# Performance work log

Hardware: AMD Instinct MI355X
Metric: run time of the kernel (lower is better)

Reference implementation:

```python
import jax, jax.numpy as jnp
import numpy as np

ALPHA = 1000.0


def setup_inputs() -> dict:
    key = jax.random.key(0)
    ks = jax.random.split(key, 5)
    B, D_in, K = 8192, 2048, 256  # K = n_clusters = embed_dim (square cluster_reps)
    x = jax.random.normal(ks[0], (B, D_in), dtype=jnp.float32)
    W_enc = jax.random.normal(ks[1], (D_in, K), dtype=jnp.float32) * (1.0 / np.sqrt(D_in))
    b_enc = jnp.zeros((K,), dtype=jnp.float32)
    W_dec = jax.random.normal(ks[2], (K, D_in), dtype=jnp.float32) * (1.0 / np.sqrt(K))
    b_dec = jnp.zeros((D_in,), dtype=jnp.float32)
    cluster_reps = jax.random.normal(ks[3], (K, K), dtype=jnp.float32)
    return {"x": x, "W_enc": W_enc, "b_enc": b_enc, "W_dec": W_dec,
            "b_dec": b_dec, "cluster_reps": cluster_reps}


def reference(x, W_enc, b_enc, W_dec, b_dec, cluster_reps):
    # Autoencoder (linear MLP stand-in for the injected module)
    emb = x @ W_enc + b_enc                    # [B, K]
    reconstruction = emb @ W_dec + b_dec       # [B, D_in]

    # Squared Euclidean distance to each cluster rep, in GEMM form: [B, K]
    # dist[b, k] = ||emb_b||^2 - 2 emb_b . c_k + ||c_k||^2
    dist = (jnp.sum(emb * emb, axis=1, keepdims=True)
            - 2.0 * (emb @ cluster_reps.T)
            + jnp.sum(cluster_reps * cluster_reps, axis=1)[None, :])

    stack_dist = dist.T                        # [K, B] (matches torch.stack over clusters)
    min_dist = jnp.min(stack_dist, axis=0)     # [B]
    stack_exp = jnp.exp(-ALPHA * (stack_dist - min_dist[None, :]))  # stable softmin
    softmax = stack_exp / jnp.sum(stack_exp, axis=0, keepdims=True)
    weighted_dist = stack_dist * softmax       # [K, B]
    return weighted_dist, reconstruction
```

## Files before the change

kernel.cpp:

```cpp
#include <hip/hip_runtime.h>

#define ALPHA_F 1000.0f

typedef _Float16 half8 __attribute__((ext_vector_type(8)));
typedef float floatx4 __attribute__((ext_vector_type(4)));

__global__ __launch_bounds__(256) void prep(
    const float* __restrict__ W_enc, const float* __restrict__ W_dec,
    const float* __restrict__ creps,
    _Float16* __restrict__ Wh, _Float16* __restrict__ Wl,
    _Float16* __restrict__ Wdh,
    _Float16* __restrict__ Ch, _Float16* __restrict__ Cl,
    float* __restrict__ cnorm)
{
    const int bid = blockIdx.x;
    if (bid < 256) {
        const int q = bid * 256 + threadIdx.x;
        const int n = q & 255, k8 = q >> 8;
        const int k = k8 * 8;
        half8 h, l;
        #pragma unroll
        for (int i = 0; i < 8; ++i) {
            const float v = W_enc[(size_t)(k + i) * 256 + n] * 256.0f;
            const _Float16 hi = (_Float16)v;
            h[i] = hi;
            l[i] = (_Float16)(v - (float)hi);
        }
        const int kc = k >> 5, nt = n >> 4;
        const int lane = (n & 15) | ((k8 & 3) << 4);
        const size_t idx = (size_t)((kc * 16 + nt) * 64 + lane) * 8;
        *(half8*)(Wh + idx) = h;
        *(half8*)(Wl + idx) = l;
    } else if (bid < 512) {
        const int q = (bid - 256) * 256 + threadIdx.x;
        const int n = q & 2047, k8 = q >> 11;
        const int k = k8 * 8;
        half8 h;
        #pragma unroll
        for (int i = 0; i < 8; ++i) h[i] = (_Float16)W_dec[(size_t)(k + i) * 2048 + n];
        const int kc = k8 >> 2, nt = n >> 4;
        const int lane = (n & 15) | ((k8 & 3) << 4);
        *(half8*)(Wdh + (size_t)((kc * 128 + nt) * 64 + lane) * 8) = h;
    } else if (bid < 544) {
        const int q = (bid - 512) * 256 + threadIdx.x;
        const int n = q & 255, j8 = q >> 8;
        const int j = j8 * 8;
        half8 h, l;
        #pragma unroll
        for (int i = 0; i < 8; ++i) {
            const float v = creps[(size_t)n * 256 + j + i];
            const _Float16 hi = (_Float16)v;
            h[i] = hi;
            l[i] = (_Float16)((v - (float)hi) * 2048.0f);
        }
        const int jc = j >> 5, nt = n >> 4;
        const int lane = (n & 15) | ((j8 & 3) << 4);
        const size_t idx = (size_t)((jc * 16 + nt) * 64 + lane) * 8;
        *(half8*)(Ch + idx) = h;
        *(half8*)(Cl + idx) = l;
    } else {
        const int wid = threadIdx.x >> 6, lane = threadIdx.x & 63;
        const int row = (bid - 544) * 4 + wid;
        const float4 v = *(const float4*)(creps + (size_t)row * 256 + lane * 4);
        float s = v.x * v.x + v.y * v.y + v.z * v.z + v.w * v.w;
        #pragma unroll
        for (int off = 32; off >= 1; off >>= 1) s += __shfl_xor(s, off, 64);
        if (lane == 0) cnorm[row] = s;
    }
}

__global__ __launch_bounds__(256) void emb_gemm(
    const float* __restrict__ x, const _Float16* __restrict__ Wh,
    const _Float16* __restrict__ Wl, float* __restrict__ P)
{
    __shared__ _Float16 Ah[2][2048], Al[2][2048];
    const int t = threadIdx.x, lane = t & 63, w = t >> 6;
    const int kk = blockIdx.x;
    const int mb = blockIdx.y;
    const int m0 = mb * 64;

    const int am = t >> 2, q = t & 3;
    const int aoff = (((am >> 4) * 64) + ((am & 15) | (q << 4))) * 8;
    const float* xP = x + (size_t)(m0 + am) * 2048 + kk * 512 + q * 8;

    const _Float16* bhP = Wh + (size_t)((kk * 256 + w * 4) * 64 + lane) * 8;
    const _Float16* blP = Wl + (size_t)((kk * 256 + w * 4) * 64 + lane) * 8;

    floatx4 acc[4][4] = {};
    half8 bh[4], bl[4];

    {
        const float4 v0 = *(const float4*)(xP);
        const float4 v1 = *(const float4*)(xP + 4);
        const float vv[8] = {v0.x, v0.y, v0.z, v0.w, v1.x, v1.y, v1.z, v1.w};
        half8 h8, l8;
        #pragma unroll
        for (int i = 0; i < 8; ++i) {
            const _Float16 hi = (_Float16)vv[i];
            h8[i] = hi;
            l8[i] = (_Float16)(vv[i] - (float)hi);
        }
        *(half8*)(&Ah[0][aoff]) = h8;
        *(half8*)(&Al[0][aoff]) = l8;
        #pragma unroll
        for (int ni = 0; ni < 4; ++ni) {
            bh[ni] = *(const half8*)(bhP + ni * 512);
            bl[ni] = *(const half8*)(blP + ni * 512);
        }
        asm volatile("s_waitcnt lgkmcnt(0)" ::: "memory");
        __builtin_amdgcn_sched_barrier(0);
        __builtin_amdgcn_s_barrier();
    }

    #pragma unroll 2
    for (int it = 0; it < 16; ++it) {
        const int buf = it & 1;

        float4 n0, n1;
        half8 nbh[4], nbl[4];
        if (it < 15) {
            n0 = *(const float4*)(xP + (it + 1) * 32);
            n1 = *(const float4*)(xP + (it + 1) * 32 + 4);
            #pragma unroll
            for (int ni = 0; ni < 4; ++ni) {
                nbh[ni] = *(const half8*)(bhP + (size_t)(it + 1) * 8192 + ni * 512);
                nbl[ni] = *(const half8*)(blP + (size_t)(it + 1) * 8192 + ni * 512);
            }
        }

        half8 ah[4], al[4];
        #pragma unroll
        for (int s = 0; s < 4; ++s) {
            ah[s] = *(const half8*)(&Ah[buf][(s * 64 + lane) * 8]);
            al[s] = *(const half8*)(&Al[buf][(s * 64 + lane) * 8]);
        }

        #pragma unroll
        for (int mi = 0; mi < 4; ++mi) {
            #pragma unroll
            for (int ni = 0; ni < 4; ++ni) {
                acc[mi][ni] = __builtin_amdgcn_mfma_f32_16x16x32_f16(ah[mi], bl[ni], acc[mi][ni], 0, 0, 0);
                acc[mi][ni] = __builtin_amdgcn_mfma_f32_16x16x32_f16(al[mi], bh[ni], acc[mi][ni], 0, 0, 0);
                acc[mi][ni] = __builtin_amdgcn_mfma_f32_16x16x32_f16(ah[mi], bh[ni], acc[mi][ni], 0, 0, 0);
            }
        }

        if (it < 15) {
            const float vv[8] = {n0.x, n0.y, n0.z, n0.w, n1.x, n1.y, n1.z, n1.w};
            half8 h8, l8;
            #pragma unroll
            for (int i = 0; i < 8; ++i) {
                const _Float16 hi = (_Float16)vv[i];
                h8[i] = hi;
                l8[i] = (_Float16)(vv[i] - (float)hi);
            }
            *(half8*)(&Ah[buf ^ 1][aoff]) = h8;
            *(half8*)(&Al[buf ^ 1][aoff]) = l8;
            #pragma unroll
            for (int ni = 0; ni < 4; ++ni) { bh[ni] = nbh[ni]; bl[ni] = nbl[ni]; }
            asm volatile("s_waitcnt lgkmcnt(0)" ::: "memory");
            __builtin_amdgcn_sched_barrier(0);
            __builtin_amdgcn_s_barrier();
        }
    }

    float* Pk = P + (size_t)kk * 2097152;
    #pragma unroll
    for (int mi = 0; mi < 4; ++mi) {
        #pragma unroll
        for (int ni = 0; ni < 4; ++ni) {
            const int col = w * 64 + ni * 16 + (lane & 15);
            const int rowBase = m0 + mi * 16 + (lane >> 4) * 4;
            #pragma unroll
            for (int r = 0; r < 4; ++r)
                Pk[(size_t)(rowBase + r) * 256 + col] = acc[mi][ni][r];
        }
    }
}

__global__ __launch_bounds__(256) void finalize(
    const float* __restrict__ P, const float* __restrict__ b_enc,
    _Float16* __restrict__ ehg, float* __restrict__ embf,
    float* __restrict__ enorm)
{
    const int t = threadIdx.x;
    const int b0 = blockIdx.x * 32;
    const int row = t >> 3, c8 = t & 7;
    const int grow = b0 + row;

    const float* p0 = P + (size_t)grow * 256 + c8 * 32;
    float4 v[8];
    #pragma unroll
    for (int i = 0; i < 8; ++i) v[i] = *(const float4*)(p0 + i * 4);
    #pragma unroll
    for (int kk = 1; kk < 4; ++kk) {
        const float* pk = p0 + (size_t)kk * 2097152;
        #pragma unroll
        for (int i = 0; i < 8; ++i) {
            const float4 a = *(const float4*)(pk + i * 4);
            v[i].x += a.x; v[i].y += a.y; v[i].z += a.z; v[i].w += a.w;
        }
    }
    const float inv = 1.0f / 256.0f;
    float e[32];
    float ssq = 0.0f;
    #pragma unroll
    for (int i = 0; i < 8; ++i) {
        const float4 b = *(const float4*)(b_enc + c8 * 32 + i * 4);
        e[i * 4 + 0] = v[i].x * inv + b.x;
        e[i * 4 + 1] = v[i].y * inv + b.y;
        e[i * 4 + 2] = v[i].z * inv + b.z;
        e[i * 4 + 3] = v[i].w * inv + b.w;
        ssq += e[i * 4 + 0] * e[i * 4 + 0];
        ssq += e[i * 4 + 1] * e[i * 4 + 1];
        ssq += e[i * 4 + 2] * e[i * 4 + 2];
        ssq += e[i * 4 + 3] * e[i * 4 + 3];
    }
    #pragma unroll
    for (int i = 0; i < 8; ++i) {
        float4 s4;
        s4.x = e[i * 4 + 0]; s4.y = e[i * 4 + 1];
        s4.z = e[i * 4 + 2]; s4.w = e[i * 4 + 3];
        *(float4*)(embf + (size_t)grow * 256 + c8 * 32 + i * 4) = s4;
    }
    #pragma unroll
    for (int oo = 0; oo < 4; ++oo) {
        const int q = c8 * 4 + oo;
        half8 h;
        #pragma unroll
        for (int i = 0; i < 8; ++i) h[i] = (_Float16)e[oo * 8 + i];
        const size_t idx = (size_t)(((grow >> 4) * 8 + (q >> 2)) * 64
                                    + ((grow & 15) | ((q & 3) << 4))) * 8;
        *(half8*)(ehg + idx) = h;
    }
    ssq += __shfl_xor(ssq, 1, 64);
    ssq += __shfl_xor(ssq, 2, 64);
    ssq += __shfl_xor(ssq, 4, 64);
    if (c8 == 0) enorm[grow] = ssq;
}

__global__ __launch_bounds__(256) void dist16(
    const float* __restrict__ embf, const _Float16* __restrict__ ch,
    const _Float16* __restrict__ cl, const float* __restrict__ enorm,
    const float* __restrict__ cnorm, float* __restrict__ out)
{
    __shared__ float D[16 * 257];
    __shared__ float MINV[16], SUMV[16];
    const int t = threadIdx.x, lane = t & 63, w = t >> 6;
    const int b0 = blockIdx.x * 16;
    const int arow16 = lane & 15, aoct = lane >> 4;

    floatx4 acc[4] = {}, accX[4] = {};
    for (int kc = 0; kc < 8; ++kc) {
        const float* fp = embf + (size_t)(b0 + arow16) * 256 + kc * 32 + aoct * 8;
        const float4 u0 = *(const float4*)(fp);
        const float4 u1 = *(const float4*)(fp + 4);
        const float vv[8] = {u0.x, u0.y, u0.z, u0.w, u1.x, u1.y, u1.z, u1.w};
        half8 ah, al;
        #pragma unroll
        for (int j = 0; j < 8; ++j) {
            const _Float16 hi = (_Float16)vv[j];
            ah[j] = hi;
            al[j] = (_Float16)((vv[j] - (float)hi) * 2048.0f);
        }
        #pragma unroll
        for (int ni = 0; ni < 4; ++ni) {
            const size_t bb = (size_t)((kc * 16 + (w * 4 + ni)) * 64 + lane) * 8;
            const half8 bh = *(const half8*)(ch + bb);
            const half8 bl = *(const half8*)(cl + bb);
            acc[ni]  = __builtin_amdgcn_mfma_f32_16x16x32_f16(ah, bh, acc[ni], 0, 0, 0);
            accX[ni] = __builtin_amdgcn_mfma_f32_16x16x32_f16(ah, bl, accX[ni], 0, 0, 0);
            accX[ni] = __builtin_amdgcn_mfma_f32_16x16x32_f16(al, bh, accX[ni], 0, 0, 0);
        }
    }

    const float invs = 1.0f / 2048.0f;
    #pragma unroll
    for (int ni = 0; ni < 4; ++ni) {
        const int k = w * 64 + ni * 16 + (lane & 15);
        const float cn = cnorm[k];
        #pragma unroll
        for (int r = 0; r < 4; ++r) {
            const int rl = (lane >> 4) * 4 + r;
            const float S = acc[ni][r] + accX[ni][r] * invs;
            D[rl * 257 + k] = enorm[b0 + rl] - 2.0f * S + cn;
        }
    }
    __syncthreads();

    #pragma unroll
    for (int rr = 0; rr < 4; ++rr) {
        const int r = w * 4 + rr;
        const float d0 = D[r * 257 + lane +   0];
        const float d1 = D[r * 257 + lane +  64];
        const float d2 = D[r * 257 + lane + 128];
        const float d3 = D[r * 257 + lane + 192];
        float mn = fminf(fminf(d0, d1), fminf(d2, d3));
        #pragma unroll
        for (int off = 32; off >= 1; off >>= 1) mn = fminf(mn, __shfl_xor(mn, off, 64));
        float s = expf(-ALPHA_F * (d0 - mn)) + expf(-ALPHA_F * (d1 - mn))
                + expf(-ALPHA_F * (d2 - mn)) + expf(-ALPHA_F * (d3 - mn));
        #pragma unroll
        for (int off = 32; off >= 1; off >>= 1) s += __shfl_xor(s, off, 64);
        if (lane == 0) { MINV[r] = mn; SUMV[r] = s; }
    }
    __syncthreads();

    const int b = t & 15, kg = t >> 4;
    const float mn = MINV[b], sv = SUMV[b];
    #pragma unroll
    for (int kk = 0; kk < 16; ++kk) {
        const int k = kk * 16 + kg;
        const float dv = D[b * 257 + k];
        out[(size_t)k * 8192 + b0 + b] = dv * expf(-ALPHA_F * (dv - mn)) / sv;
    }
}

__global__ __launch_bounds__(256) void recon_gemm(
    const _Float16* __restrict__ embh, const _Float16* __restrict__ Wdh,
    const float* __restrict__ b_dec, float* __restrict__ out)
{
    const int t = threadIdx.x, lane = t & 63, w = t >> 6;
    const int wm = w >> 1, wn = w & 1;
    const int nb = blockIdx.x, mb = blockIdx.y;

    floatx4 acc[4][4] = {};

    #pragma unroll
    for (int kc = 0; kc < 8; ++kc) {
        half8 a[4], b[4];
        #pragma unroll
        for (int mi = 0; mi < 4; ++mi)
            a[mi] = *(const half8*)(embh + (size_t)(((mb * 8 + wm * 4 + mi) * 8 + kc) * 64 + lane) * 8);
        #pragma unroll
        for (int ni = 0; ni < 4; ++ni)
            b[ni] = *(const half8*)(Wdh + (size_t)((kc * 128 + nb * 8 + wn * 4 + ni) * 64 + lane) * 8);
        #pragma unroll
        for (int mi = 0; mi < 4; ++mi)
            #pragma unroll
            for (int ni = 0; ni < 4; ++ni)
                acc[mi][ni] = __builtin_amdgcn_mfma_f32_16x16x32_f16(a[mi], b[ni], acc[mi][ni], 0, 0, 0);
    }

    #pragma unroll
    for (int ni = 0; ni < 4; ++ni) {
        const int col = nb * 128 + (wn * 4 + ni) * 16 + (lane & 15);
        const float bias = b_dec[col];
        #pragma unroll
        for (int mi = 0; mi < 4; ++mi) {
            const int rowBase = mb * 128 + (wm * 4 + mi) * 16 + (lane >> 4) * 4;
            #pragma unroll
            for (int r = 0; r < 4; ++r)
                out[(size_t)(rowBase + r) * 2048 + col] = acc[mi][ni][r] + bias;
        }
    }
}

extern "C" void kernel_launch(void* const* d_in, const int* in_sizes, int n_in,
                              void* d_out, int out_size, void* d_ws, size_t ws_size,
                              hipStream_t stream) {
    const float* x     = (const float*)d_in[0];
    const float* W_enc = (const float*)d_in[1];
    const float* b_enc = (const float*)d_in[2];
    const float* W_dec = (const float*)d_in[3];
    const float* b_dec = (const float*)d_in[4];
    const float* creps = (const float*)d_in[5];

    float* out_w   = (float*)d_out;
    float* out_rec = out_w + (size_t)256 * 8192;
    float* P       = out_rec;

    float*     cnorm = (float*)d_ws;
    _Float16*  embh  = (_Float16*)(cnorm + 256);
    _Float16*  Whf   = embh + (size_t)8192 * 256;
    _Float16*  Wlf   = Whf + (size_t)2048 * 256;
    _Float16*  Wdh   = Wlf + (size_t)2048 * 256;
    _Float16*  crh   = Wdh + (size_t)256 * 2048;
    _Float16*  crl   = crh + (size_t)256 * 256;
    float*     enorm = (float*)(crl + (size_t)256 * 256);
    float*     embf  = enorm + 8192;

    prep<<<608, 256, 0, stream>>>(W_enc, W_dec, creps, Whf, Wlf, Wdh, crh, crl, cnorm);

    emb_gemm<<<dim3(4, 128), 256, 0, stream>>>(x, Whf, Wlf, P);

    finalize<<<256, 256, 0, stream>>>(P, b_enc, embh, embf, enorm);

    dist16<<<512, 256, 0, stream>>>(embf, crh, crl, enorm, cnorm, out_w);

    recon_gemm<<<dim3(16, 64), 256, 0, stream>>>(embh, Wdh, b_dec, out_rec);
}
```

Measured before the change: 195.9 us.

## Fuse split-K finalize into distance kernel, removing embf/enorm round trip

Merges the split-K reduction, bias add, norm computation and fp16 embedding packing into the distance/softmin kernel. Each block reduces the four P partials for its 16 rows directly into registers, computes the row norms via shuffles and shared memory, and writes the fp16 embedding for the reconstruction GEMM. This removes one kernel launch and the global fp32 embedding and norm buffers. In exchange, all four waves redundantly read the same partial sums, and register pressure rises from holding 64 floats per thread.

```diff
diff --git a/kernel.cpp b/kernel.cpp
--- a/kernel.cpp
+++ b/kernel.cpp
@@ -178,90 +178,71 @@
     }
 }
 
-__global__ __launch_bounds__(256) void finalize(
+__global__ __launch_bounds__(256) void dist_fused(
     const float* __restrict__ P, const float* __restrict__ b_enc,
-    _Float16* __restrict__ ehg, float* __restrict__ embf,
-    float* __restrict__ enorm)
-{
-    const int t = threadIdx.x;
-    const int b0 = blockIdx.x * 32;
-    const int row = t >> 3, c8 = t & 7;
-    const int grow = b0 + row;
-
-    const float* p0 = P + (size_t)grow * 256 + c8 * 32;
-    float4 v[8];
-    #pragma unroll
-    for (int i = 0; i < 8; ++i) v[i] = *(const float4*)(p0 + i * 4);
-    #pragma unroll
-    for (int kk = 1; kk < 4; ++kk) {
-        const float* pk = p0 + (size_t)kk * 2097152;
-        #pragma unroll
-        for (int i = 0; i < 8; ++i) {
-            const float4 a = *(const float4*)(pk + i * 4);
-            v[i].x += a.x; v[i].y += a.y; v[i].z += a.z; v[i].w += a.w;
-        }
-    }
-    const float inv = 1.0f / 256.0f;
-    float e[32];
-    float ssq = 0.0f;
-    #pragma unroll
-    for (int i = 0; i < 8; ++i) {
-        const float4 b = *(const float4*)(b_enc + c8 * 32 + i * 4);
-        e[i * 4 + 0] = v[i].x * inv + b.x;
-        e[i * 4 + 1] = v[i].y * inv + b.y;
-        e[i * 4 + 2] = v[i].z * inv + b.z;
-        e[i * 4 + 3] = v[i].w * inv + b.w;
-        ssq += e[i * 4 + 0] * e[i * 4 + 0];
-        ssq += e[i * 4 + 1] * e[i * 4 + 1];
-        ssq += e[i * 4 + 2] * e[i * 4 + 2];
-        ssq += e[i * 4 + 3] * e[i * 4 + 3];
-    }
-    #pragma unroll
-    for (int i = 0; i < 8; ++i) {
-        float4 s4;
-        s4.x = e[i * 4 + 0]; s4.y = e[i * 4 + 1];
-        s4.z = e[i * 4 + 2]; s4.w = e[i * 4 + 3];
-        *(float4*)(embf + (size_t)grow * 256 + c8 * 32 + i * 4) = s4;
-    }
-    #pragma unroll
-    for (int oo = 0; oo < 4; ++oo) {
-        const int q = c8 * 4 + oo;
-        half8 h;
-        #pragma unroll
-        for (int i = 0; i < 8; ++i) h[i] = (_Float16)e[oo * 8 + i];
-        const size_t idx = (size_t)(((grow >> 4) * 8 + (q >> 2)) * 64
-                                    + ((grow & 15) | ((q & 3) << 4))) * 8;
-        *(half8*)(ehg + idx) = h;
-    }
-    ssq += __shfl_xor(ssq, 1, 64);
-    ssq += __shfl_xor(ssq, 2, 64);
-    ssq += __shfl_xor(ssq, 4, 64);
-    if (c8 == 0) enorm[grow] = ssq;
-}
-
-__global__ __launch_bounds__(256) void dist16(
-    const float* __restrict__ embf, const _Float16* __restrict__ ch,
-    const _Float16* __restrict__ cl, const float* __restrict__ enorm,
-    const float* __restrict__ cnorm, float* __restrict__ out)
+    const _Float16* __restrict__ ch, const _Float16* __restrict__ cl,
+    const float* __restrict__ cnorm,
+    _Float16* __restrict__ ehg, float* __restrict__ out)
 {
     __shared__ float D[16 * 257];
+    __shared__ float ENORM[16];
     __shared__ float MINV[16], SUMV[16];
     const int t = threadIdx.x, lane = t & 63, w = t >> 6;
-    const int b0 = blockIdx.x * 16;
+    const int blk = blockIdx.x;
+    const int b0 = blk * 16;
     const int arow16 = lane & 15, aoct = lane >> 4;
 
+    float e[8][8];
+    float ssq = 0.0f;
+    const float inv = 1.0f / 256.0f;
+    #pragma unroll
+    for (int kc = 0; kc < 8; ++kc) {
+        const float* p0 = P + (size_t)(b0 + arow16) * 256 + kc * 32 + aoct * 8;
+        float4 v0 = *(const float4*)(p0);
+        float4 v1 = *(const float4*)(p0 + 4);
+        #pragma unroll
+        for (int kkp = 1; kkp < 4; ++kkp) {
+            const float* pk = p0 + (size_t)kkp * 2097152;
+            const float4 a0 = *(const float4*)(pk);
+            const float4 a1 = *(const float4*)(pk + 4);
+            v0.x += a0.x; v0.y += a0.y; v0.z += a0.z; v0.w += a0.w;
+            v1.x += a1.x; v1.y += a1.y; v1.z += a1.z; v1.w += a1.w;
+        }
+        const float4 bb0 = *(const float4*)(b_enc + kc * 32 + aoct * 8);
+        const float4 bb1 = *(const float4*)(b_enc + kc * 32 + aoct * 8 + 4);
+        e[kc][0] = v0.x * inv + bb0.x;
+        e[kc][1] = v0.y * inv + bb0.y;
+        e[kc][2] = v0.z * inv + bb0.z;
+        e[kc][3] = v0.w * inv + bb0.w;
+        e[kc][4] = v1.x * inv + bb1.x;
+        e[kc][5] = v1.y * inv + bb1.y;
+        e[kc][6] = v1.z * inv + bb1.z;
+        e[kc][7] = v1.w * inv + bb1.w;
+        #pragma unroll
+        for (int j = 0; j < 8; ++j) ssq += e[kc][j] * e[kc][j];
+    }
+    #pragma unroll
+    for (int kq = 0; kq < 2; ++kq) {
+        const int kc = w * 2 + kq;
+        half8 h;
+        #pragma unroll
+        for (int j = 0; j < 8; ++j) h[j] = (_Float16)e[kc][j];
+        *(half8*)(ehg + (size_t)(((blk * 8 + kc) * 64) + lane) * 8) = h;
+    }
+    ssq += __shfl_xor(ssq, 16, 64);
+    ssq += __shfl_xor(ssq, 32, 64);
+    if (t < 16) ENORM[t] = ssq;
+    __syncthreads();
+
     floatx4 acc[4] = {}, accX[4] = {};
+    #pragma unroll
     for (int kc = 0; kc < 8; ++kc) {
-        const float* fp = embf + (size_t)(b0 + arow16) * 256 + kc * 32 + aoct * 8;
-        const float4 u0 = *(const float4*)(fp);
-        const float4 u1 = *(const float4*)(fp + 4);
-        const float vv[8] = {u0.x, u0.y, u0.z, u0.w, u1.x, u1.y, u1.z, u1.w};
         half8 ah, al;
         #pragma unroll
         for (int j = 0; j < 8; ++j) {
-            const _Float16 hi = (_Float16)vv[j];
+            const _Float16 hi = (_Float16)e[kc][j];
             ah[j] = hi;
-            al[j] = (_Float16)((vv[j] - (float)hi) * 2048.0f);
+            al[j] = (_Float16)((e[kc][j] - (float)hi) * 2048.0f);
         }
         #pragma unroll
         for (int ni = 0; ni < 4; ++ni) {
@@ -283,7 +264,7 @@
         for (int r = 0; r < 4; ++r) {
             const int rl = (lane >> 4) * 4 + r;
             const float S = acc[ni][r] + accX[ni][r] * invs;
-            D[rl * 257 + k] = enorm[b0 + rl] - 2.0f * S + cn;
+            D[rl * 257 + k] = ENORM[rl] - 2.0f * S + cn;
         }
     }
     __syncthreads();
@@ -377,16 +358,12 @@
     _Float16*  Wdh   = Wlf + (size_t)2048 * 256;
     _Float16*  crh   = Wdh + (size_t)256 * 2048;
     _Float16*  crl   = crh + (size_t)256 * 256;
-    float*     enorm = (float*)(crl + (size_t)256 * 256);
-    float*     embf  = enorm + 8192;
 
     prep<<<608, 256, 0, stream>>>(W_enc, W_dec, creps, Whf, Wlf, Wdh, crh, crl, cnorm);
 
     emb_gemm<<<dim3(4, 128), 256, 0, stream>>>(x, Whf, Wlf, P);
 
-    finalize<<<256, 256, 0, stream>>>(P, b_enc, embh, embf, enorm);
-
-    dist16<<<512, 256, 0, stream>>>(embf, crh, crl, enorm, cnorm, out_w);
+    dist_fused<<<512, 256, 0, stream>>>(P, b_enc, crh, crl, cnorm, embh, out_w);
 
     recon_gemm<<<dim3(16, 64), 256, 0, stream>>>(embh, Wdh, b_dec, out_rec);
 }
```

New measurement: 200.1 us. +2.1%, slower.
